# Kernel tuning notes

Hardware: AMD Instinct MI355X
Metric: run time of the kernel (lower is better)

The kernel has to match this reference:

```python
import jax, jax.numpy as jnp
import numpy as np

N = 100000      # nodes
E = 1600000     # edges
G = 64          # graphs in batch
H = 128         # hidden (== num_features)
L = 4           # num_layers
C = 16          # num_classes
NCAND = 100000  # candidate edges
BN_EPS = 1e-5


def setup_inputs() -> dict:
    key = jax.random.key(0)
    ks = jax.random.split(key, 24)
    s = 0.05
    inp = {}
    inp["x"] = jax.random.normal(ks[0], (N, H), dtype=jnp.float32)
    inp["edge_index"] = jax.random.randint(ks[1], (2, E), 0, N)
    inp["batch"] = jnp.sort(jax.random.randint(ks[2], (N,), 0, G))
    inp["candidate_edges"] = jax.random.randint(ks[3], (2, NCAND), 0, N)
    # GIN conv params, stacked over L layers (all layers are H->H since num_features==hidden)
    inp["cW1"] = jax.random.normal(ks[4], (L, H, H), dtype=jnp.float32) * s
    inp["cb1"] = jnp.zeros((L, H), jnp.float32)
    inp["cW2"] = jax.random.normal(ks[5], (L, H, H), dtype=jnp.float32) * s
    inp["cb2"] = jnp.zeros((L, H), jnp.float32)
    inp["cgamma"] = jnp.ones((L, H), jnp.float32)
    inp["cbeta"] = jnp.zeros((L, H), jnp.float32)
    inp["ceps"] = jnp.zeros((L,), jnp.float32)  # train_eps=True, init 0
    # node classifier: L*H -> 2H -> H -> H -> C (dropout is identity in eval)
    inp["ncW1"] = jax.random.normal(ks[6], (L * H, 2 * H), dtype=jnp.float32) * s
    inp["ncb1"] = jnp.zeros((2 * H,), jnp.float32)
    inp["ncW2"] = jax.random.normal(ks[7], (2 * H, H), dtype=jnp.float32) * s
    inp["ncb2"] = jnp.zeros((H,), jnp.float32)
    inp["ncW3"] = jax.random.normal(ks[8], (H, H), dtype=jnp.float32) * s
    inp["ncb3"] = jnp.zeros((H,), jnp.float32)
    inp["ncW4"] = jax.random.normal(ks[9], (H, C), dtype=jnp.float32) * s
    inp["ncb4"] = jnp.zeros((C,), jnp.float32)
    # edge predictor: 2*L*H -> 2H -> H -> 1
    inp["epW1"] = jax.random.normal(ks[10], (2 * L * H, 2 * H), dtype=jnp.float32) * s
    inp["epb1"] = jnp.zeros((2 * H,), jnp.float32)
    inp["epW2"] = jax.random.normal(ks[11], (2 * H, H), dtype=jnp.float32) * s
    inp["epb2"] = jnp.zeros((H,), jnp.float32)
    inp["epW3"] = jax.random.normal(ks[12], (H, 1), dtype=jnp.float32) * s
    inp["epb3"] = jnp.zeros((1,), jnp.float32)
    return inp


def _forward(x, cW1, cb1, cW2, cb2, cgamma, cbeta, ceps,
             ncW1, ncb1, ncW2, ncb2, ncW3, ncb3, ncW4, ncb4,
             epW1, epb1, epW2, epb2, epW3, epb3,
             edge_index, batch, candidate_edges):
    src, dst = edge_index[0], edge_index[1]
    h = x
    xs = []
    for l in range(L):
        # GIN: (1+eps)*x_i + sum_{j->i} x_j  (scatter-add over destination nodes)
        agg = jax.ops.segment_sum(h[src], dst, num_segments=N)
        z = (1.0 + ceps[l]) * h + agg
        z = jax.nn.relu(z @ cW1[l] + cb1[l])
        z = jax.nn.relu(z @ cW2[l] + cb2[l])
        # BatchNorm1d (training-mode batch statistics, biased variance)
        mu = z.mean(axis=0)
        var = jnp.var(z, axis=0)
        h = (z - mu) * jax.lax.rsqrt(var + BN_EPS) * cgamma[l] + cbeta[l]
        xs.append(h)
    emb = jnp.concatenate(xs, axis=-1)  # [N, L*H]
    # global mean pool over graphs
    sums = jax.ops.segment_sum(emb, batch, num_segments=G)
    cnt = jax.ops.segment_sum(jnp.ones((N, 1), emb.dtype), batch, num_segments=G)
    gemb = sums / jnp.maximum(cnt, 1.0)  # [G, L*H]
    t = jax.nn.relu(gemb @ ncW1 + ncb1)
    t = jax.nn.relu(t @ ncW2 + ncb2)
    t = jax.nn.relu(t @ ncW3 + ncb3)
    class_output = jax.nn.log_softmax(t @ ncW4 + ncb4, axis=1)  # [G, C]
    # link prediction: gather node embeddings per candidate edge
    ef = jnp.concatenate([emb[candidate_edges[0]], emb[candidate_edges[1]]], axis=1)  # [NC, 2*L*H]
    u = jax.nn.relu(ef @ epW1 + epb1)
    u = jax.nn.relu(u @ epW2 + epb2)
    edge_scores = jax.nn.sigmoid((u @ epW3 + epb3).squeeze(-1))  # [NC]
    return class_output, edge_scores


def reference(x, cW1, cb1, cW2, cb2, cgamma, cbeta, ceps,
              ncW1, ncb1, ncW2, ncb2, ncW3, ncb3, ncW4, ncb4,
              epW1, epb1, epW2, epb2, epW3, epb3,
              edge_index, batch, candidate_edges):
    return _forward(x, cW1, cb1, cW2, cb2, cgamma, cbeta, ceps,
                    ncW1, ncb1, ncW2, ncb2, ncW3, ncb3, ncW4, ncb4,
                    epW1, epb1, epW2, epb2, epW3, epb3,
                    edge_index, batch, candidate_edges)
```

## Files before the change

### kernel.cpp

```cpp
#include <hip/hip_runtime.h>
#include <math.h>

#define NN 100000
#define EE 1600000
#define GG 64
#define HH 128
#define LL 4
#define CCLS 16
#define NC 100000
#define NB 49
#define LDK 40
#define LDA2 136
#define LDC 260

typedef __attribute__((ext_vector_type(8))) short bf16x8;
typedef __attribute__((ext_vector_type(4))) float f32x4;

__device__ __forceinline__ unsigned short f2bf(float x) {
  union { float f; unsigned int u; } v; v.f = x;
  unsigned int r = v.u + 0x7fffu + ((v.u >> 16) & 1u);
  return (unsigned short)(r >> 16);
}
__device__ __forceinline__ float bl(unsigned u) {
  union { unsigned u; float f; } v; v.u = u << 16; return v.f;
}
__device__ __forceinline__ float bh(unsigned u) {
  union { unsigned u; float f; } v; v.u = u & 0xffff0000u; return v.f;
}

__global__ void hist_kernel(const int* __restrict__ dst, int* __restrict__ cnt, int E) {
  int i = (blockIdx.x * 256 + threadIdx.x) * 4;
  if (i + 3 < E) {
    int4 v = *(const int4*)(dst + i);
    atomicAdd(&cnt[v.x], 1);
    atomicAdd(&cnt[v.y], 1);
    atomicAdd(&cnt[v.z], 1);
    atomicAdd(&cnt[v.w], 1);
  } else {
    for (int k = i; k < E; ++k) atomicAdd(&cnt[dst[k]], 1);
  }
}

__global__ __launch_bounds__(256) void scan_p1(const int* __restrict__ cnt,
                                               int* __restrict__ bsum, int n) {
  __shared__ int red[256];
  int tid = threadIdx.x;
  int base = blockIdx.x * 1024 + tid * 4;
  int s = 0;
  if (base + 3 < n) {
    int4 v = *(const int4*)(cnt + base);
    s = v.x + v.y + v.z + v.w;
  } else {
    for (int i = 0; i < 4; ++i) if (base + i < n) s += cnt[base + i];
  }
  red[tid] = s;
  __syncthreads();
  for (int st = 128; st >= 1; st >>= 1) {
    if (tid < st) red[tid] += red[tid + st];
    __syncthreads();
  }
  if (tid == 0) bsum[blockIdx.x] = red[0];
}

__global__ void scan_p2(int* __restrict__ bsum, int* __restrict__ rowptr,
                        int* __restrict__ bcursor, int nb, int n) {
  __shared__ int buf[128];
  int tid = threadIdx.x;
  int v = (tid < nb) ? bsum[tid] : 0;
  buf[tid] = v;
  __syncthreads();
  for (int off = 1; off < 128; off <<= 1) {
    int t = (tid >= off) ? buf[tid - off] : 0;
    __syncthreads();
    buf[tid] += t;
    __syncthreads();
  }
  if (tid < nb) bsum[tid] = buf[tid] - v;
  if (tid == 127) rowptr[n] = buf[127];
  __syncthreads();
  if (tid < NB) bcursor[tid] = bsum[2 * tid];
}

__global__ __launch_bounds__(256) void scan_p3(const int* __restrict__ cnt,
                                               const int* __restrict__ bsum,
                                               int* __restrict__ rowptr,
                                               int* __restrict__ cursor, int n) {
  __shared__ int red[256];
  int tid = threadIdx.x;
  int base = blockIdx.x * 1024 + tid * 4;
  int v[4] = {0, 0, 0, 0};
  if (base + 3 < n) {
    int4 t = *(const int4*)(cnt + base);
    v[0] = t.x; v[1] = t.y; v[2] = t.z; v[3] = t.w;
  } else {
    for (int i = 0; i < 4; ++i) if (base + i < n) v[i] = cnt[base + i];
  }
  int s = v[0] + v[1] + v[2] + v[3];
  red[tid] = s;
  __syncthreads();
  for (int off = 1; off < 256; off <<= 1) {
    int t = (tid >= off) ? red[tid - off] : 0;
    __syncthreads();
    red[tid] += t;
    __syncthreads();
  }
  int run = bsum[blockIdx.x] + red[tid] - s;
  int4 o;
  o.x = run; o.y = run + v[0]; o.z = o.y + v[1]; o.w = o.z + v[2];
  if (base + 3 < n) {
    *(int4*)(rowptr + base) = o;
    *(int4*)(cursor + base) = o;
  } else {
    int oo[4] = {o.x, o.y, o.z, o.w};
    for (int i = 0; i < 4; ++i)
      if (base + i < n) { rowptr[base + i] = oo[i]; cursor[base + i] = oo[i]; }
  }
}

__global__ __launch_bounds__(256) void partition_kernel(const int* __restrict__ src,
                                                        const int* __restrict__ dst,
                                                        int* __restrict__ bcursor,
                                                        int2* __restrict__ pairs, int E) {
  __shared__ int sS[4096];
  __shared__ int sD[4096];
  __shared__ int hist[NB];
  __shared__ int base[NB];
  int tid = threadIdx.x;
  int base_e = blockIdx.x * 4096;
  int cnt = min(4096, E - base_e);
  if (tid < NB) hist[tid] = 0;
  for (int i = tid * 4; i < cnt; i += 1024) {
    if (i + 3 < cnt) {
      *(int4*)(sS + i) = *(const int4*)(src + base_e + i);
      *(int4*)(sD + i) = *(const int4*)(dst + base_e + i);
    } else {
      for (int k = i; k < cnt; ++k) { sS[k] = src[base_e + k]; sD[k] = dst[base_e + k]; }
    }
  }
  __syncthreads();
  for (int i = tid; i < cnt; i += 256) atomicAdd(&hist[sD[i] >> 11], 1);
  __syncthreads();
  if (tid < NB) {
    base[tid] = atomicAdd(&bcursor[tid], hist[tid]);
    hist[tid] = 0;
  }
  __syncthreads();
  for (int i = tid; i < cnt; i += 256) {
    int d = sD[i];
    int b = d >> 11;
    int off = atomicAdd(&hist[b], 1);
    pairs[base[b] + off] = make_int2(sS[i], d);
  }
}

__global__ __launch_bounds__(256) void scatter_csr(const int2* __restrict__ pairs,
                                                   const int* __restrict__ rowptr,
                                                   int* __restrict__ cursor,
                                                   int* __restrict__ csr_src) {
  int b = blockIdx.x % 56;
  int slice = blockIdx.x / 56;
  if (b >= NB) return;
  int start = rowptr[b * 2048];
  int endn = min((b + 1) * 2048, NN);
  int end = rowptr[endn];
  for (int i = start + slice * 256 + threadIdx.x; i < end; i += 8 * 256) {
    int2 p = pairs[i];
    int pos = atomicAdd(&cursor[p.y], 1);
    csr_src[pos] = p.x;
  }
}

#define NF2B (NN * HH / 4)
#define NCVW (LL * 16384 + 32768)
__global__ void convert_all(const float* __restrict__ x, unsigned short* __restrict__ x16,
                            const float* __restrict__ cW1, const float* __restrict__ cW2,
                            unsigned short* __restrict__ WT1, unsigned short* __restrict__ WT2,
                            const float* __restrict__ epW2, unsigned short* __restrict__ W2T) {
  int gi = blockIdx.x * 256 + threadIdx.x;
  if (gi < NF2B) {
    float4 v = ((const float4*)x)[gi];
    unsigned short r[4] = {f2bf(v.x), f2bf(v.y), f2bf(v.z), f2bf(v.w)};
    *(uint2*)(x16 + (size_t)gi * 4) = *(uint2*)r;
    return;
  }
  int idx = gi - NF2B;
  if (idx < LL * 16384) {
    int l = idx >> 14, r = idx & 16383, k = r >> 7, n = r & 127;
    WT1[l * 16384 + n * 128 + k] = f2bf(cW1[idx]);
    WT2[l * 16384 + n * 128 + k] = f2bf(cW2[idx]);
  } else if (idx < NCVW) {
    int j = idx - LL * 16384;
    int k = j >> 7, n = j & 127;
    W2T[(size_t)n * 256 + k] = f2bf(epW2[j]);
  }
}

__global__ __launch_bounds__(256) void ep_w1_prep(
    const float* __restrict__ epW1, const float* __restrict__ epb1,
    const float* __restrict__ bnsum, const float* __restrict__ bnsumsq,
    const float* __restrict__ gamma, const float* __restrict__ beta,
    unsigned short* __restrict__ W1T, float* __restrict__ b1x) {
  __shared__ float red[256];
  int n = blockIdx.x;
  int tid = threadIdx.x;
  const float inv_n = 1.0f / (float)NN;
  int k0 = tid * 4;
  unsigned short w16[4];
  float part = 0.f;
#pragma unroll
  for (int j = 0; j < 4; ++j) {
    int k = k0 + j;
    int c = k & 511;
    float mu = bnsum[c] * inv_n;
    float var = bnsumsq[c] * inv_n - mu * mu;
    float s = rsqrtf(var + 1e-5f) * gamma[c];
    float o = beta[c] - s * mu;
    float w = epW1[(size_t)k * 256 + n];
    w16[j] = f2bf(s * w);
    part += o * w;
  }
  *(uint2*)(W1T + (size_t)n * 1024 + k0) = *(uint2*)w16;
  red[tid] = part;
  __syncthreads();
  for (int st = 128; st >= 1; st >>= 1) {
    if (tid < st) red[tid] += red[tid + st];
    __syncthreads();
  }
  if (tid == 0) b1x[n] = epb1[n] + red[0];
}

__global__ __launch_bounds__(256, 8) void aggregate_bf16(
    const unsigned short* __restrict__ h16, int ld,
    const int* __restrict__ rowptr,
    const int* __restrict__ csr_src,
    const float* __restrict__ ceps_l,
    const float* __restrict__ bnsum_prev,
    const float* __restrict__ bnsumsq_prev,
    const float* __restrict__ gamma_prev,
    const float* __restrict__ beta_prev,
    unsigned short* __restrict__ out, int n) {
  int wave = threadIdx.x >> 6;
  int lane = threadIdx.x & 63;
  int sub = lane >> 4;
  int li = lane & 15;
  int node = blockIdx.x * 16 + wave * 4 + sub;
  if (node >= n) return;
  int c8 = li * 8;
  float acc[8] = {};
  int b = rowptr[node], e = rowptr[node + 1];
  int j = b;
  for (; j + 4 <= e; j += 4) {
    uint4 u[4];
#pragma unroll
    for (int t = 0; t < 4; ++t) {
      int s = csr_src[j + t];
      u[t] = *(const uint4*)(h16 + (size_t)s * ld + c8);
    }
#pragma unroll
    for (int t = 0; t < 4; ++t) {
      acc[0] += bl(u[t].x); acc[1] += bh(u[t].x);
      acc[2] += bl(u[t].y); acc[3] += bh(u[t].y);
      acc[4] += bl(u[t].z); acc[5] += bh(u[t].z);
      acc[6] += bl(u[t].w); acc[7] += bh(u[t].w);
    }
  }
  for (; j < e; ++j) {
    int s = csr_src[j];
    uint4 u = *(const uint4*)(h16 + (size_t)s * ld + c8);
    acc[0] += bl(u.x); acc[1] += bh(u.x);
    acc[2] += bl(u.y); acc[3] += bh(u.y);
    acc[4] += bl(u.z); acc[5] += bh(u.z);
    acc[6] += bl(u.w); acc[7] += bh(u.w);
  }
  float eps1 = 1.0f + *ceps_l;
  uint4 hu = *(const uint4*)(h16 + (size_t)node * ld + c8);
  acc[0] = fmaf(eps1, bl(hu.x), acc[0]); acc[1] = fmaf(eps1, bh(hu.x), acc[1]);
  acc[2] = fmaf(eps1, bl(hu.y), acc[2]); acc[3] = fmaf(eps1, bh(hu.y), acc[3]);
  acc[4] = fmaf(eps1, bl(hu.z), acc[4]); acc[5] = fmaf(eps1, bh(hu.z), acc[5]);
  acc[6] = fmaf(eps1, bl(hu.w), acc[6]); acc[7] = fmaf(eps1, bh(hu.w), acc[7]);
  float degw = (float)(e - b) + eps1;
  unsigned short o[8];
  if (bnsum_prev) {
    const float inv_n = 1.0f / (float)NN;
#pragma unroll
    for (int k = 0; k < 8; ++k) {
      int c = c8 + k;
      float mu = bnsum_prev[c] * inv_n;
      float var = bnsumsq_prev[c] * inv_n - mu * mu;
      float s = rsqrtf(var + 1e-5f) * gamma_prev[c];
      float off = beta_prev[c] - s * mu;
      o[k] = f2bf(fmaf(s, acc[k], degw * off));
    }
  } else {
#pragma unroll
    for (int k = 0; k < 8; ++k) o[k] = f2bf(acc[k]);
  }
  *(uint4*)(out + (size_t)node * 128 + c8) = *(uint4*)o;
}

__global__ __launch_bounds__(256) void trunk_fused(
    const unsigned short* __restrict__ A16,
    const unsigned short* __restrict__ W1T, const float* __restrict__ b1,
    const unsigned short* __restrict__ W2T, const float* __restrict__ b2,
    float* __restrict__ bnsum, float* __restrict__ bnsumsq,
    unsigned short* __restrict__ C16 , int M) {
  __shared__ unsigned short As[128 * LDA2];
  __shared__ unsigned short Bs[128 * LDA2];
  const int tid = threadIdx.x;
  const int bm = blockIdx.x * 128;
  const int lane = tid & 63;
  const int wave = tid >> 6;
  const int wr = (wave >> 1) << 6;
  const int wc = (wave & 1) << 6;
  const int ar = tid >> 1;
  const int ah = (tid & 1) << 4;
  int gra = bm + ar; if (gra >= M) gra = M - 1;
  const unsigned short* Arow = A16 + (size_t)gra * 128;
  const unsigned short* B1row = W1T + (size_t)ar * 128;
  const int mrow = lane & 15;
  const int kq = (lane >> 4) << 3;

  {
    uint4 aR[8], bR[8];
#pragma unroll
    for (int i = 0; i < 4; ++i) {
      aR[2 * i]     = *(const uint4*)(Arow + (i << 5) + ah);
      aR[2 * i + 1] = *(const uint4*)(Arow + (i << 5) + ah + 8);
      bR[2 * i]     = *(const uint4*)(B1row + (i << 5) + ah);
      bR[2 * i + 1] = *(const uint4*)(B1row + (i << 5) + ah + 8);
    }
#pragma unroll
    for (int i = 0; i < 4; ++i) {
      *(uint4*)(As + ar * LDA2 + (i << 5) + ah)     = aR[2 * i];
      *(uint4*)(As + ar * LDA2 + (i << 5) + ah + 8) = aR[2 * i + 1];
      *(uint4*)(Bs + ar * LDA2 + (i << 5) + ah)     = bR[2 * i];
      *(uint4*)(Bs + ar * LDA2 + (i << 5) + ah + 8) = bR[2 * i + 1];
    }
  }
  f32x4 acc[4][4] = {};
  __syncthreads();
#pragma unroll
  for (int ks = 0; ks < 4; ++ks) {
    const int k0 = ks << 5;
    bf16x8 af[4], bfv[4];
#pragma unroll
    for (int t = 0; t < 4; ++t)
      af[t] = *(const bf16x8*)(As + (wr + t * 16 + mrow) * LDA2 + k0 + kq);
#pragma unroll
    for (int t = 0; t < 4; ++t)
      bfv[t] = *(const bf16x8*)(Bs + (wc + t * 16 + mrow) * LDA2 + k0 + kq);
#pragma unroll
    for (int mt = 0; mt < 4; ++mt)
#pragma unroll
      for (int nt = 0; nt < 4; ++nt)
        acc[mt][nt] = __builtin_amdgcn_mfma_f32_16x16x32_bf16(af[mt], bfv[nt], acc[mt][nt], 0, 0, 0);
  }
  uint4 w2[8];
  {
    const unsigned short* B2row = W2T + (size_t)ar * 128;
#pragma unroll
    for (int i = 0; i < 4; ++i) {
      w2[2 * i]     = *(const uint4*)(B2row + (i << 5) + ah);
      w2[2 * i + 1] = *(const uint4*)(B2row + (i << 5) + ah + 8);
    }
  }
  __syncthreads();
  const int crow = (lane >> 4) << 2;
  const int ccol = lane & 15;
#pragma unroll
  for (int nt = 0; nt < 4; ++nt) {
    int c = wc + nt * 16 + ccol;
    float bz = b1[c];
#pragma unroll
    for (int mt = 0; mt < 4; ++mt) {
      int rl = wr + mt * 16 + crow;
#pragma unroll
      for (int i = 0; i < 4; ++i)
        As[(rl + i) * LDA2 + c] = f2bf(fmaxf(acc[mt][nt][i] + bz, 0.f));
    }
  }
#pragma unroll
  for (int i = 0; i < 4; ++i) {
    *(uint4*)(Bs + ar * LDA2 + (i << 5) + ah)     = w2[2 * i];
    *(uint4*)(Bs + ar * LDA2 + (i << 5) + ah + 8) = w2[2 * i + 1];
  }
#pragma unroll
  for (int mt = 0; mt < 4; ++mt)
#pragma unroll
    for (int nt = 0; nt < 4; ++nt)
      acc[mt][nt] = (f32x4){0.f, 0.f, 0.f, 0.f};
  __syncthreads();
#pragma unroll
  for (int ks = 0; ks < 4; ++ks) {
    const int k0 = ks << 5;
    bf16x8 af[4], bfv[4];
#pragma unroll
    for (int t = 0; t < 4; ++t)
      af[t] = *(const bf16x8*)(As + (wr + t * 16 + mrow) * LDA2 + k0 + kq);
#pragma unroll
    for (int t = 0; t < 4; ++t)
      bfv[t] = *(const bf16x8*)(Bs + (wc + t * 16 + mrow) * LDA2 + k0 + kq);
#pragma unroll
    for (int mt = 0; mt < 4; ++mt)
#pragma unroll
      for (int nt = 0; nt < 4; ++nt)
        acc[mt][nt] = __builtin_amdgcn_mfma_f32_16x16x32_bf16(af[mt], bfv[nt], acc[mt][nt], 0, 0, 0);
  }
  __syncthreads();
#pragma unroll
  for (int nt = 0; nt < 4; ++nt) {
    int c = wc + nt * 16 + ccol;
    float bz = b2[c];
    float s = 0.f, q = 0.f;
#pragma unroll
    for (int mt = 0; mt < 4; ++mt) {
      int rl = wr + mt * 16 + crow;
      int rbase = bm + rl;
#pragma unroll
      for (int i = 0; i < 4; ++i) {
        float v = fmaxf(acc[mt][nt][i] + bz, 0.f);
        Bs[(rl + i) * LDA2 + c] = f2bf(v);
        if (rbase + i < M) { s += v; q += v * v; }
      }
    }
    s += __shfl_xor(s, 16, 64);
    s += __shfl_xor(s, 32, 64);
    q += __shfl_xor(q, 16, 64);
    q += __shfl_xor(q, 32, 64);
    if (lane < 16) {
      atomicAdd(&bnsum[c], s);
      atomicAdd(&bnsumsq[c], q);
    }
  }
  __syncthreads();
#pragma unroll
  for (int p = 0; p < 8; ++p) {
    int r = p * 16 + (tid >> 4);
    int q8 = (tid & 15) * 8;
    if (bm + r < M)
      *(uint4*)(C16 + (size_t)(bm + r) * 512 + q8) =
          *(const uint4*)(Bs + r * LDA2 + q8);
  }
}

__global__ __launch_bounds__(512, 4) void ep_fused(
    const unsigned short* __restrict__ emb16, const int* __restrict__ cand,
    const unsigned short* __restrict__ W1T ,
    const float* __restrict__ b1,
    const unsigned short* __restrict__ W2T ,
    const float* __restrict__ b2, const float* __restrict__ epW3,
    const float* __restrict__ epb3,
    float* __restrict__ out, int M) {
  __shared__ unsigned short smem[128 * LDC];
  __shared__ float sDotA[128];
  __shared__ float sDotB[128];
  unsigned short* const As0 = smem;
  unsigned short* const As1 = smem + 128 * LDK;
  unsigned short* const Bs0 = smem + 2 * 128 * LDK;
  unsigned short* const Bs1 = smem + 2 * 128 * LDK + 256 * LDK;
  const int tid = threadIdx.x;
  const int bm = blockIdx.x * 128;
  const int lane = tid & 63;
  const int wave = tid >> 6;
  const int wr = (wave >> 2) << 6;
  const int wc = (wave & 3) << 6;
  f32x4 acc[4][4] = {};
  const int ar = tid >> 2;
  const int ah = (tid & 3) << 3;
  int gra = bm + ar; if (gra >= M) gra = M - 1;
  const int node0 = cand[gra];
  const int node1 = cand[NC + gra];
  const int br = tid >> 1;
  const int bh8 = (tid & 1) << 4;
  const unsigned short* Brow = W1T + (size_t)br * 1024 + bh8;
  const unsigned short* Arow0 = emb16 + (size_t)node0 * 512 + ah;
  const unsigned short* Arow1 = emb16 + (size_t)node1 * 512 + ah - 512;
  const int mrow = lane & 15;
  const int kq = (lane >> 4) << 3;

  auto ldA = [&](int k) -> uint4 {
    const unsigned short* p = (k < 16) ? Arow0 : Arow1;
    return *(const uint4*)(p + (k << 5));
  };
  auto ldB0v = [&](int k) -> uint4 { return *(const uint4*)(Brow + (k << 5)); };
  auto ldB1v = [&](int k) -> uint4 { return *(const uint4*)(Brow + (k << 5) + 8); };
  auto stTile = [&](unsigned short* Ab, unsigned short* Bb, uint4 a, uint4 x0, uint4 x1) {
    *(uint4*)(Ab + ar * LDK + ah) = a;
    *(uint4*)(Bb + br * LDK + bh8) = x0;
    *(uint4*)(Bb + br * LDK + bh8 + 8) = x1;
  };
  auto mma_step = [&](const unsigned short* A, const unsigned short* B) {
    bf16x8 af[4], bfv[4];
#pragma unroll
    for (int t = 0; t < 4; ++t)
      af[t] = *(const bf16x8*)(A + (wr + t * 16 + mrow) * LDK + kq);
#pragma unroll
    for (int t = 0; t < 4; ++t)
      bfv[t] = *(const bf16x8*)(B + (wc + t * 16 + mrow) * LDK + kq);
#pragma unroll
    for (int mt = 0; mt < 4; ++mt)
#pragma unroll
      for (int nt = 0; nt < 4; ++nt)
        acc[mt][nt] = __builtin_amdgcn_mfma_f32_16x16x32_bf16(af[mt], bfv[nt], acc[mt][nt], 0, 0, 0);
  };

  uint4 aA, aB, b0, b1v;
  {
    uint4 a0 = ldA(0), x0 = ldB0v(0), x1 = ldB1v(0);
    stTile(As0, Bs0, a0, x0, x1);
    aA = ldA(1); b0 = ldB0v(1); b1v = ldB1v(1);
    aB = ldA(2);
  }
  __syncthreads();
  for (int it = 0; it < 16; ++it) {
    const int s0 = 2 * it;
    stTile(As1, Bs1, aA, b0, b1v);
    if (s0 + 3 < 32) aA = ldA(s0 + 3);
    if (s0 + 2 < 32) { b0 = ldB0v(s0 + 2); b1v = ldB1v(s0 + 2); }
    mma_step(As0, Bs0);
    __syncthreads();
    const int s1 = s0 + 1;
    if (s1 < 31) {
      stTile(As0, Bs0, aB, b0, b1v);
      if (s1 + 3 < 32) aB = ldA(s1 + 3);
      if (s1 + 2 < 32) { b0 = ldB0v(s1 + 2); b1v = ldB1v(s1 + 2); }
    }
    mma_step(As1, Bs1);
    __syncthreads();
  }

  const int crow = (lane >> 4) << 2;
  const int ccol = lane & 15;
#pragma unroll
  for (int nt = 0; nt < 4; ++nt) {
    int c = wc + nt * 16 + ccol;
    float bz = b1[c];
#pragma unroll
    for (int mt = 0; mt < 4; ++mt) {
      int rl = wr + mt * 16 + crow;
#pragma unroll
      for (int i = 0; i < 4; ++i)
        smem[(rl + i) * LDC + c] = f2bf(fmaxf(acc[mt][nt][i] + bz, 0.f));
    }
  }
  __syncthreads();
  const int wr2 = (wave >> 1) << 5;
  const int wc2 = (wave & 1) << 6;
  f32x4 acc2[2][4] = {};
  for (int ks = 0; ks < 8; ++ks) {
    const int k0 = ks << 5;
    bf16x8 af[2], bfv[4];
#pragma unroll
    for (int t = 0; t < 2; ++t)
      af[t] = *(const bf16x8*)(smem + (wr2 + t * 16 + mrow) * LDC + k0 + kq);
#pragma unroll
    for (int t = 0; t < 4; ++t)
      bfv[t] = *(const bf16x8*)(W2T + (size_t)(wc2 + t * 16 + mrow) * 256 + k0 + kq);
#pragma unroll
    for (int mt = 0; mt < 2; ++mt)
#pragma unroll
      for (int nt = 0; nt < 4; ++nt)
        acc2[mt][nt] = __builtin_amdgcn_mfma_f32_16x16x32_bf16(af[mt], bfv[nt], acc2[mt][nt], 0, 0, 0);
  }
  float w3v[4], bz2[4];
#pragma unroll
  for (int nt = 0; nt < 4; ++nt) {
    int c = wc2 + nt * 16 + ccol;
    w3v[nt] = epW3[c];
    bz2[nt] = b2[c];
  }
  float* sBank = (wave & 1) ? sDotB : sDotA;
#pragma unroll
  for (int mt = 0; mt < 2; ++mt) {
#pragma unroll
    for (int i = 0; i < 4; ++i) {
      int rl = wr2 + mt * 16 + crow + i;
      float p = 0.f;
#pragma unroll
      for (int nt = 0; nt < 4; ++nt)
        p = fmaf(fmaxf(acc2[mt][nt][i] + bz2[nt], 0.f), w3v[nt], p);
      p += __shfl_xor(p, 1, 64);
      p += __shfl_xor(p, 2, 64);
      p += __shfl_xor(p, 4, 64);
      p += __shfl_xor(p, 8, 64);
      if ((lane & 15) == 0) sBank[rl] = p;
    }
  }
  __syncthreads();
  if (tid < 128) {
    int r = bm + tid;
    if (r < M) out[r] = 1.f / (1.f + expf(-(sDotA[tid] + sDotB[tid] + epb3[0])));
  }
}

__global__ __launch_bounds__(256) void pool_bf16(const unsigned short* __restrict__ emb16,
                                                 const int* __restrict__ batch,
                                                 float* __restrict__ gsum) {
  __shared__ int se[2];
  __shared__ float sRed[512];
  int g = blockIdx.x;
  int chunk = blockIdx.y;
  int tid = threadIdx.x;
  if (tid < 2) {
    int x = g + tid;
    int lo = 0, hi = NN;
    while (lo < hi) {
      int mid = (lo + hi) >> 1;
      if (batch[mid] < x) lo = mid + 1; else hi = mid;
    }
    se[tid] = lo;
  }
  __syncthreads();
  int s = se[0], e = se[1];
  int len = e - s;
  int per = (len + 7) >> 3;
  int r0 = s + chunk * per;
  int r1 = min(r0 + per, e);
  int c8 = (tid & 63) * 8;
  int wgrp = tid >> 6;
  float acc[8] = {};
  for (int r = r0 + wgrp; r < r1; r += 4) {
    uint4 u = *(const uint4*)(emb16 + (size_t)r * 512 + c8);
    acc[0] += bl(u.x); acc[1] += bh(u.x);
    acc[2] += bl(u.y); acc[3] += bh(u.y);
    acc[4] += bl(u.z); acc[5] += bh(u.z);
    acc[6] += bl(u.w); acc[7] += bh(u.w);
  }
  if (wgrp == 0) {
#pragma unroll
    for (int j = 0; j < 8; ++j) sRed[c8 + j] = acc[j];
  }
  __syncthreads();
  for (int w = 1; w < 4; ++w) {
    if (wgrp == w) {
#pragma unroll
      for (int j = 0; j < 8; ++j) sRed[c8 + j] += acc[j];
    }
    __syncthreads();
  }
  if (r0 < r1 && tid < 128) {
#pragma unroll
    for (int j = 0; j < 4; ++j)
      atomicAdd(&gsum[g * 512 + tid * 4 + j], sRed[tid * 4 + j]);
  }
}

__global__ __launch_bounds__(256) void nc_fused(
    const float* __restrict__ gsum, const int* __restrict__ batch,
    const float* __restrict__ bnsum, const float* __restrict__ bnsumsq,
    const float* __restrict__ gamma, const float* __restrict__ beta,
    const float* __restrict__ W1, const float* __restrict__ b1,
    const float* __restrict__ W2, const float* __restrict__ b2,
    const float* __restrict__ W3, const float* __restrict__ b3,
    const float* __restrict__ W4, const float* __restrict__ b4,
    float* __restrict__ out) {
  __shared__ float row[512];
  __shared__ float t1[256];
  __shared__ float t2[128];
  __shared__ float t3s[128];
  __shared__ float lg[16];
  __shared__ int se[2];
  int g = blockIdx.x;
  int tid = threadIdx.x;
  if (tid < 2) {
    int x = g + tid;
    int lo = 0, hi = NN;
    while (lo < hi) {
      int mid = (lo + hi) >> 1;
      if (batch[mid] < x) lo = mid + 1; else hi = mid;
    }
    se[tid] = lo;
  }
  __syncthreads();
  float inv = 1.0f / fmaxf((float)(se[1] - se[0]), 1.0f);
  const float inv_n = 1.0f / (float)NN;
#pragma unroll
  for (int h = 0; h < 2; ++h) {
    int c = tid + h * 256;
    float mu = bnsum[c] * inv_n;
    float var = bnsumsq[c] * inv_n - mu * mu;
    float s = rsqrtf(var + 1e-5f) * gamma[c];
    float o = beta[c] - s * mu;
    row[c] = fmaf(gsum[g * 512 + c] * inv, s, o);
  }
  __syncthreads();
  {
    float acc = b1[tid];
#pragma unroll 8
    for (int k = 0; k < 512; ++k) acc = fmaf(row[k], W1[k * 256 + tid], acc);
    t1[tid] = fmaxf(acc, 0.f);
  }
  __syncthreads();
  if (tid < 128) {
    float acc = b2[tid];
#pragma unroll 8
    for (int k = 0; k < 256; ++k) acc = fmaf(t1[k], W2[k * 128 + tid], acc);
    t2[tid] = fmaxf(acc, 0.f);
  }
  __syncthreads();
  if (tid < 128) {
    float acc = b3[tid];
#pragma unroll 8
    for (int k = 0; k < 128; ++k) acc = fmaf(t2[k], W3[k * 128 + tid], acc);
    t3s[tid] = fmaxf(acc, 0.f);
  }
  __syncthreads();
  if (tid < 16) {
    float acc = b4[tid];
#pragma unroll 8
    for (int k = 0; k < 128; ++k) acc = fmaf(t3s[k], W4[k * 16 + tid], acc);
    lg[tid] = acc;
  }
  __syncthreads();
  if (tid < 16) {
    float v = lg[tid];
    float m = v;
    for (int j = 0; j < 16; ++j) m = fmaxf(m, lg[j]);
    float s = 0.f;
    for (int j = 0; j < 16; ++j) s += expf(lg[j] - m);
    out[g * 16 + tid] = v - m - logf(s);
  }
}

extern "C" void kernel_launch(void* const* d_in, const int* in_sizes, int n_in,
                              void* d_out, int out_size, void* d_ws, size_t ws_size,
                              hipStream_t stream) {
  const float* x = (const float*)d_in[0];
  const int* edge_index = (const int*)d_in[1];
  const int* batch = (const int*)d_in[2];
  const int* cand = (const int*)d_in[3];
  const float* cW1 = (const float*)d_in[4];
  const float* cb1 = (const float*)d_in[5];
  const float* cW2 = (const float*)d_in[6];
  const float* cb2 = (const float*)d_in[7];
  const float* cgamma = (const float*)d_in[8];
  const float* cbeta = (const float*)d_in[9];
  const float* ceps = (const float*)d_in[10];
  const float* ncW1 = (const float*)d_in[11];
  const float* ncb1 = (const float*)d_in[12];
  const float* ncW2 = (const float*)d_in[13];
  const float* ncb2 = (const float*)d_in[14];
  const float* ncW3 = (const float*)d_in[15];
  const float* ncb3 = (const float*)d_in[16];
  const float* ncW4 = (const float*)d_in[17];
  const float* ncb4 = (const float*)d_in[18];
  const float* epW1 = (const float*)d_in[19];
  const float* epb1 = (const float*)d_in[20];
  const float* epW2 = (const float*)d_in[21];
  const float* epb2 = (const float*)d_in[22];
  const float* epW3 = (const float*)d_in[23];
  const float* epb3 = (const float*)d_in[24];

  char* ws = (char*)d_ws;
  size_t off = 0;
  auto alloc = [&](size_t bytes) -> void* {
    off = (off + 255) & ~(size_t)255;
    void* p = ws + off;
    off += bytes;
    return p;
  };
  size_t zz_bytes = (size_t)NN * 4 + 512 * 4 + 512 * 4 + (size_t)GG * 512 * 4;
  char* zz = (char*)alloc(zz_bytes);
  int* cnt = (int*)zz;
  float* bnsum = (float*)(zz + (size_t)NN * 4);
  float* bnsumsq = bnsum + 512;
  float* gsum = bnsumsq + 512;
  int* rowptr = (int*)alloc((size_t)(NN + 1) * 4);
  int* cursor = (int*)alloc((size_t)NN * 4);
  int* csr_src = (int*)alloc((size_t)EE * 4);
  int2* pairs = (int2*)alloc((size_t)EE * 8);
  int* bsum = (int*)alloc(128 * 4);
  int* bcursor = (int*)alloc(64 * 4);
  unsigned short* x16 = (unsigned short*)alloc((size_t)NN * 128 * 2);
  unsigned short* g16a = (unsigned short*)alloc((size_t)NN * 128 * 2);
  unsigned short* emb16 = (unsigned short*)alloc((size_t)NN * 512 * 2);
  unsigned short* WT1 = (unsigned short*)alloc((size_t)LL * 16384 * 2);
  unsigned short* WT2 = (unsigned short*)alloc((size_t)LL * 16384 * 2);
  unsigned short* W1T = (unsigned short*)alloc((size_t)1024 * 256 * 2);
  unsigned short* W2T = (unsigned short*)alloc((size_t)256 * 128 * 2);
  float* b1x = (float*)alloc(256 * 4);

  const int* esrc = edge_index;
  const int* edst = edge_index + EE;
  const int nblk = (NN + 1023) / 1024;
  const int nech = (EE + 4095) / 4096;

  hipMemsetAsync(zz, 0, zz_bytes, stream);
  hist_kernel<<<(EE / 4 + 255) / 256, 256, 0, stream>>>(edst, cnt, EE);
  scan_p1<<<nblk, 256, 0, stream>>>(cnt, bsum, NN);
  scan_p2<<<1, 128, 0, stream>>>(bsum, rowptr, bcursor, nblk, NN);
  scan_p3<<<nblk, 256, 0, stream>>>(cnt, bsum, rowptr, cursor, NN);
  partition_kernel<<<nech, 256, 0, stream>>>(esrc, edst, bcursor, pairs, EE);
  scatter_csr<<<56 * 8, 256, 0, stream>>>(pairs, rowptr, cursor, csr_src);
  convert_all<<<(NF2B + NCVW + 255) / 256, 256, 0, stream>>>(
      x, x16, cW1, cW2, WT1, WT2, epW2, W2T);

  for (int l = 0; l < LL; ++l) {
    const unsigned short* h16 = (l == 0) ? x16 : (emb16 + (size_t)(l - 1) * 128);
    int ld = (l == 0) ? 128 : 512;
    aggregate_bf16<<<(NN + 15) / 16, 256, 0, stream>>>(
        h16, ld, rowptr, csr_src, ceps + l,
        (l == 0) ? nullptr : bnsum + (l - 1) * 128,
        (l == 0) ? nullptr : bnsumsq + (l - 1) * 128,
        (l == 0) ? nullptr : cgamma + (l - 1) * 128,
        (l == 0) ? nullptr : cbeta + (l - 1) * 128,
        g16a, NN);
    trunk_fused<<<(NN + 127) / 128, 256, 0, stream>>>(
        g16a, WT1 + (size_t)l * 16384, cb1 + l * 128,
        WT2 + (size_t)l * 16384, cb2 + l * 128,
        bnsum + l * 128, bnsumsq + l * 128, emb16 + (size_t)l * 128, NN);
  }
  ep_w1_prep<<<256, 256, 0, stream>>>(epW1, epb1, bnsum, bnsumsq, cgamma, cbeta,
                                      W1T, b1x);

  pool_bf16<<<dim3(GG, 8), 256, 0, stream>>>(emb16, batch, gsum);
  nc_fused<<<GG, 256, 0, stream>>>(gsum, batch, bnsum, bnsumsq, cgamma, cbeta,
                                   ncW1, ncb1, ncW2, ncb2, ncW3, ncb3,
                                   ncW4, ncb4, (float*)d_out);

  ep_fused<<<(NC + 127) / 128, 512, 0, stream>>>(
      emb16, cand, W1T, b1x, W2T, epb2, epW3, epb3,
      (float*)d_out + GG * CCLS, NC);
}
```

Measured before the change: 953.2 us.

## Fuse neighbor aggregation into the trunk MLP kernel, writing aggregates to LDS

Each 128-row trunk block now gathers neighbor features for its own nodes and writes the bf16 aggregates straight into shared memory. This replaces the separate aggregate kernel and its global intermediate buffer. It removes one launch per layer and a write plus re-read of the 100000x128 bf16 intermediate. In exchange, the gather runs with far fewer blocks (782 instead of 6250), without the occupancy hint, and with higher register/LDS pressure, so memory-latency hiding for the random gathers may suffer.

```diff
diff --git a/kernel.cpp b/kernel.cpp
--- a/kernel.cpp
+++ b/kernel.cpp
@@ -229,77 +229,12 @@
   if (tid == 0) b1x[n] = epb1[n] + red[0];
 }
 
-__global__ __launch_bounds__(256, 8) void aggregate_bf16(
+__global__ __launch_bounds__(256) void layer_fused(
     const unsigned short* __restrict__ h16, int ld,
-    const int* __restrict__ rowptr,
-    const int* __restrict__ csr_src,
+    const int* __restrict__ rowptr, const int* __restrict__ csr_src,
     const float* __restrict__ ceps_l,
-    const float* __restrict__ bnsum_prev,
-    const float* __restrict__ bnsumsq_prev,
-    const float* __restrict__ gamma_prev,
-    const float* __restrict__ beta_prev,
-    unsigned short* __restrict__ out, int n) {
-  int wave = threadIdx.x >> 6;
-  int lane = threadIdx.x & 63;
-  int sub = lane >> 4;
-  int li = lane & 15;
-  int node = blockIdx.x * 16 + wave * 4 + sub;
-  if (node >= n) return;
-  int c8 = li * 8;
-  float acc[8] = {};
-  int b = rowptr[node], e = rowptr[node + 1];
-  int j = b;
-  for (; j + 4 <= e; j += 4) {
-    uint4 u[4];
-#pragma unroll
-    for (int t = 0; t < 4; ++t) {
-      int s = csr_src[j + t];
-      u[t] = *(const uint4*)(h16 + (size_t)s * ld + c8);
-    }
-#pragma unroll
-    for (int t = 0; t < 4; ++t) {
-      acc[0] += bl(u[t].x); acc[1] += bh(u[t].x);
-      acc[2] += bl(u[t].y); acc[3] += bh(u[t].y);
-      acc[4] += bl(u[t].z); acc[5] += bh(u[t].z);
-      acc[6] += bl(u[t].w); acc[7] += bh(u[t].w);
-    }
-  }
-  for (; j < e; ++j) {
-    int s = csr_src[j];
-    uint4 u = *(const uint4*)(h16 + (size_t)s * ld + c8);
-    acc[0] += bl(u.x); acc[1] += bh(u.x);
-    acc[2] += bl(u.y); acc[3] += bh(u.y);
-    acc[4] += bl(u.z); acc[5] += bh(u.z);
-    acc[6] += bl(u.w); acc[7] += bh(u.w);
-  }
-  float eps1 = 1.0f + *ceps_l;
-  uint4 hu = *(const uint4*)(h16 + (size_t)node * ld + c8);
-  acc[0] = fmaf(eps1, bl(hu.x), acc[0]); acc[1] = fmaf(eps1, bh(hu.x), acc[1]);
-  acc[2] = fmaf(eps1, bl(hu.y), acc[2]); acc[3] = fmaf(eps1, bh(hu.y), acc[3]);
-  acc[4] = fmaf(eps1, bl(hu.z), acc[4]); acc[5] = fmaf(eps1, bh(hu.z), acc[5]);
-  acc[6] = fmaf(eps1, bl(hu.w), acc[6]); acc[7] = fmaf(eps1, bh(hu.w), acc[7]);
-  float degw = (float)(e - b) + eps1;
-  unsigned short o[8];
-  if (bnsum_prev) {
-    const float inv_n = 1.0f / (float)NN;
-#pragma unroll
-    for (int k = 0; k < 8; ++k) {
-      int c = c8 + k;
-      float mu = bnsum_prev[c] * inv_n;
-      float var = bnsumsq_prev[c] * inv_n - mu * mu;
-      float s = rsqrtf(var + 1e-5f) * gamma_prev[c];
-      float off = beta_prev[c] - s * mu;
-      o[k] = f2bf(fmaf(s, acc[k], degw * off));
-    }
-  } else {
-#pragma unroll
-    for (int k = 0; k < 8; ++k) o[k] = f2bf(acc[k]);
-  }
-  *(uint4*)(out + (size_t)node * 128 + c8) = *(uint4*)o;
-}
-
-__global__ __launch_bounds__(256) void trunk_fused(
-    const unsigned short* __restrict__ A16,
+    const float* __restrict__ bnsum_prev, const float* __restrict__ bnsumsq_prev,
+    const float* __restrict__ gamma_prev, const float* __restrict__ beta_prev,
     const unsigned short* __restrict__ W1T, const float* __restrict__ b1,
     const unsigned short* __restrict__ W2T, const float* __restrict__ b2,
     float* __restrict__ bnsum, float* __restrict__ bnsumsq,
@@ -314,27 +249,84 @@
   const int wc = (wave & 1) << 6;
   const int ar = tid >> 1;
   const int ah = (tid & 1) << 4;
-  int gra = bm + ar; if (gra >= M) gra = M - 1;
-  const unsigned short* Arow = A16 + (size_t)gra * 128;
   const unsigned short* B1row = W1T + (size_t)ar * 128;
   const int mrow = lane & 15;
   const int kq = (lane >> 4) << 3;
 
   {
-    uint4 aR[8], bR[8];
+    uint4 bR[8];
 #pragma unroll
     for (int i = 0; i < 4; ++i) {
-      aR[2 * i]     = *(const uint4*)(Arow + (i << 5) + ah);
-      aR[2 * i + 1] = *(const uint4*)(Arow + (i << 5) + ah + 8);
       bR[2 * i]     = *(const uint4*)(B1row + (i << 5) + ah);
       bR[2 * i + 1] = *(const uint4*)(B1row + (i << 5) + ah + 8);
     }
 #pragma unroll
     for (int i = 0; i < 4; ++i) {
-      *(uint4*)(As + ar * LDA2 + (i << 5) + ah)     = aR[2 * i];
-      *(uint4*)(As + ar * LDA2 + (i << 5) + ah + 8) = aR[2 * i + 1];
       *(uint4*)(Bs + ar * LDA2 + (i << 5) + ah)     = bR[2 * i];
       *(uint4*)(Bs + ar * LDA2 + (i << 5) + ah + 8) = bR[2 * i + 1];
+    }
+  }
+  {
+    const int sg = tid >> 4;
+    const int li = tid & 15;
+    const int c8 = li * 8;
+    float eps1 = 1.0f + *ceps_l;
+    float scv[8], offv[8];
+    if (bnsum_prev) {
+      const float inv_n = 1.0f / (float)NN;
+#pragma unroll
+      for (int k = 0; k < 8; ++k) {
+        int c = c8 + k;
+        float mu = bnsum_prev[c] * inv_n;
+        float var = bnsumsq_prev[c] * inv_n - mu * mu;
+        float s = rsqrtf(var + 1e-5f) * gamma_prev[c];
+        scv[k] = s;
+        offv[k] = beta_prev[c] - s * mu;
+      }
+    } else {
+#pragma unroll
+      for (int k = 0; k < 8; ++k) { scv[k] = 1.f; offv[k] = 0.f; }
+    }
+    for (int it = 0; it < 8; ++it) {
+      int nodeLocal = it * 16 + sg;
+      int node = bm + nodeLocal;
+      if (node >= M) node = M - 1;
+      int b0 = rowptr[node], e0 = rowptr[node + 1];
+      float acc[8] = {};
+      int j = b0;
+      for (; j + 4 <= e0; j += 4) {
+        uint4 u[4];
+#pragma unroll
+        for (int t = 0; t < 4; ++t) {
+          int s = csr_src[j + t];
+          u[t] = *(const uint4*)(h16 + (size_t)s * ld + c8);
+        }
+#pragma unroll
+        for (int t = 0; t < 4; ++t) {
+          acc[0] += bl(u[t].x); acc[1] += bh(u[t].x);
+          acc[2] += bl(u[t].y); acc[3] += bh(u[t].y);
+          acc[4] += bl(u[t].z); acc[5] += bh(u[t].z);
+          acc[6] += bl(u[t].w); acc[7] += bh(u[t].w);
+        }
+      }
+      for (; j < e0; ++j) {
+        int s = csr_src[j];
+        uint4 u = *(const uint4*)(h16 + (size_t)s * ld + c8);
+        acc[0] += bl(u.x); acc[1] += bh(u.x);
+        acc[2] += bl(u.y); acc[3] += bh(u.y);
+        acc[4] += bl(u.z); acc[5] += bh(u.z);
+        acc[6] += bl(u.w); acc[7] += bh(u.w);
+      }
+      uint4 hu = *(const uint4*)(h16 + (size_t)node * ld + c8);
+      acc[0] = fmaf(eps1, bl(hu.x), acc[0]); acc[1] = fmaf(eps1, bh(hu.x), acc[1]);
+      acc[2] = fmaf(eps1, bl(hu.y), acc[2]); acc[3] = fmaf(eps1, bh(hu.y), acc[3]);
+      acc[4] = fmaf(eps1, bl(hu.z), acc[4]); acc[5] = fmaf(eps1, bh(hu.z), acc[5]);
+      acc[6] = fmaf(eps1, bl(hu.w), acc[6]); acc[7] = fmaf(eps1, bh(hu.w), acc[7]);
+      float degw = (float)(e0 - b0) + eps1;
+      unsigned short o[8];
+#pragma unroll
+      for (int i = 0; i < 8; ++i) o[i] = f2bf(fmaf(scv[i], acc[i], degw * offv[i]));
+      *(uint4*)(As + nodeLocal * LDA2 + c8) = *(uint4*)o;
     }
   }
   f32x4 acc[4][4] = {};
@@ -772,7 +764,6 @@
   int* bsum = (int*)alloc(128 * 4);
   int* bcursor = (int*)alloc(64 * 4);
   unsigned short* x16 = (unsigned short*)alloc((size_t)NN * 128 * 2);
-  unsigned short* g16a = (unsigned short*)alloc((size_t)NN * 128 * 2);
   unsigned short* emb16 = (unsigned short*)alloc((size_t)NN * 512 * 2);
   unsigned short* WT1 = (unsigned short*)alloc((size_t)LL * 16384 * 2);
   unsigned short* WT2 = (unsigned short*)alloc((size_t)LL * 16384 * 2);
@@ -798,15 +789,13 @@
   for (int l = 0; l < LL; ++l) {
     const unsigned short* h16 = (l == 0) ? x16 : (emb16 + (size_t)(l - 1) * 128);
     int ld = (l == 0) ? 128 : 512;
-    aggregate_bf16<<<(NN + 15) / 16, 256, 0, stream>>>(
+    layer_fused<<<(NN + 127) / 128, 256, 0, stream>>>(
         h16, ld, rowptr, csr_src, ceps + l,
         (l == 0) ? nullptr : bnsum + (l - 1) * 128,
         (l == 0) ? nullptr : bnsumsq + (l - 1) * 128,
         (l == 0) ? nullptr : cgamma + (l - 1) * 128,
         (l == 0) ? nullptr : cbeta + (l - 1) * 128,
-        g16a, NN);
-    trunk_fused<<<(NN + 127) / 128, 256, 0, stream>>>(
-        g16a, WT1 + (size_t)l * 16384, cb1 + l * 128,
+        WT1 + (size_t)l * 16384, cb1 + l * 128,
         WT2 + (size_t)l * 16384, cb2 + l * 128,
         bnsum + l * 128, bnsumsq + l * 128, emb16 + (size_t)l * 128, NN);
   }
```

After: 1.038 ms. 1.09x slower.
